# Kernel optimization log

Hardware: AMD Instinct MI355X
Metric: run time of the kernel (lower is better)

The kernel has to match this reference:

```python
import jax, jax.numpy as jnp
import numpy as np

N, D, S, K = 4096, 256, 32, 4   # nodes, in_dim(=out_dim), subspace_dim, num_heads
ETA = 0.5
LAMBDA_SPARSE = 0.05
EDGE_P = 0.02  # graph density for the random adjacency mask


def setup_inputs() -> dict:
    key = jax.random.key(0)
    k1, k2, k3 = jax.random.split(key, 3)
    H = jax.random.normal(k1, (N, D), dtype=jnp.float32)
    # binary adjacency mask with self-loops, stored as float (matches torch usage)
    mask = (jax.random.uniform(k2, (N, N)) < EDGE_P).astype(jnp.float32)
    adj_mask = jnp.maximum(mask, jnp.eye(N, dtype=jnp.float32))
    # per-head orthonormal subspace bases U[k] = qr(randn(D,S)) -> [K, D, S]
    raw = jax.random.normal(k3, (K, D, S), dtype=jnp.float32)
    U, _ = jnp.linalg.qr(raw)
    log_precision = jnp.zeros((K, S), dtype=jnp.float32)
    threshold = jnp.full((D,), LAMBDA_SPARSE, dtype=jnp.float32)
    return {"H": H, "adj_mask": adj_mask, "U": U,
            "log_precision": log_precision, "threshold": threshold}


def reference(H, adj_mask, U, log_precision, threshold):
    s = U.shape[-1]
    inv_sqrt_s = 1.0 / jnp.sqrt(jnp.asarray(s, dtype=H.dtype))
    neg = (1.0 - adj_mask) * (-1e9)  # [N, N] additive mask

    # scan over heads keeps peak memory at one [N,N] score matrix at a time
    def head_step(agg, xs):
        Uk, lpk = xs                       # [D,S], [S]
        Z = H @ Uk                         # [N,S]  (= Zk^T in the torch code)
        Zs = Z * jnp.exp(lpk)              # precision-scaled
        scores = (Zs @ Z.T) * inv_sqrt_s + neg   # [N,N]
        alpha = jax.nn.softmax(scores, axis=-1)
        agg = agg + (alpha @ Z) @ Uk.T     # [N,D] == (Uk @ (Zk @ alpha^T))^T
        return agg, None

    agg, _ = jax.lax.scan(head_step, jnp.zeros_like(H), (U, log_precision))
    H_half = H + ETA * agg                 # in_dim == out_dim -> no proj

    # soft threshold
    H_out = jnp.sign(H_half) * jax.nn.relu(jnp.abs(H_half) - threshold[None, :])

    # orthogonality loss: sum_k ||Uk^T Uk - I||_F^2 + sum_{k<l} ||Uk^T Ul||_F^2
    C = jnp.einsum('kda,ldb->klab', U, U)  # [K,K,S,S] gram blocks (K,S small)
    Kh = U.shape[0]
    I = jnp.eye(s, dtype=U.dtype)
    diag_blocks = C[jnp.arange(Kh), jnp.arange(Kh)]          # [K,S,S]
    orth_loss = ((diag_blocks - I) ** 2).sum()
    upper = jnp.triu(jnp.ones((Kh, Kh), dtype=U.dtype), 1)[:, :, None, None]
    orth_loss = orth_loss + ((C ** 2) * upper).sum()
    return H_out, orth_loss
```

## Files before the change

kernel.cpp:

```cpp
#include <hip/hip_runtime.h>
#include <math.h>

constexpr int NN = 4096;
constexpr int DD = 256;
constexpr int SS = 32;
constexpr int KK = 4;
constexpr int MAXN = 192;
constexpr int SEGMAX = 96;
constexpr float ETA = 0.5f;

#define MEMFENCE() __asm__ volatile("" ::: "memory")

typedef float nfloat4 __attribute__((ext_vector_type(4)));

__device__ __forceinline__ float4 ntload4(const float4* p) {
  nfloat4 v = __builtin_nontemporal_load((const nfloat4*)p);
  float4 r; r.x = v.x; r.y = v.y; r.z = v.z; r.w = v.w;
  return r;
}

__global__ __launch_bounds__(256) void prep_kernel(
    const float* __restrict__ H, const float* __restrict__ U,
    const float* __restrict__ lp, float* __restrict__ Z,
    float* __restrict__ elp, float* __restrict__ lossp) {
  __shared__ float Hl[16][DD];
  __shared__ float red[4];
  const int tid = threadIdx.x;

  if (blockIdx.x < 1024) {
    const int k = blockIdx.x & 3;
    const int n0 = (blockIdx.x >> 2) * 16;

    const float4* H4 = (const float4*)(H + (size_t)n0 * DD);
    float4* Hl4 = (float4*)&Hl[0][0];
    for (int i = tid; i < 16 * DD / 4; i += 256) Hl4[i] = H4[i];
    __syncthreads();

    const int s = tid & 31;
    const int n_l = (tid >> 5) & 7;
    const float* Uk = U + (size_t)k * DD * SS;
    float acc0 = 0.f, acc1 = 0.f;
#pragma unroll 4
    for (int dq = 0; dq < DD / 4; dq++) {
      const float4 h0 = Hl4[n_l * (DD / 4) + dq];
      const float4 h1 = Hl4[(n_l + 8) * (DD / 4) + dq];
      const float u0 = Uk[(4 * dq + 0) * SS + s];
      const float u1 = Uk[(4 * dq + 1) * SS + s];
      const float u2 = Uk[(4 * dq + 2) * SS + s];
      const float u3 = Uk[(4 * dq + 3) * SS + s];
      acc0 += h0.x * u0 + h0.y * u1 + h0.z * u2 + h0.w * u3;
      acc1 += h1.x * u0 + h1.y * u1 + h1.z * u2 + h1.w * u3;
    }
    Z[((size_t)k * NN + n0 + n_l) * SS + s] = acc0;
    Z[((size_t)k * NN + n0 + n_l + 8) * SS + s] = acc1;
  } else {
    const int pair = blockIdx.x - 1024;
    if (pair == 0 && tid < KK * SS) elp[tid] = expf(lp[tid]);
    const int pk[10] = {0, 0, 0, 0, 1, 1, 1, 2, 2, 3};
    const int pl[10] = {0, 1, 2, 3, 1, 2, 3, 2, 3, 3};
    const int k = pk[pair], l = pl[pair];
    const int b = tid & 31;
    const int a0 = tid >> 5;
    float acc[4] = {0.f, 0.f, 0.f, 0.f};
    for (int d = 0; d < DD; d++) {
      const float ub = U[((size_t)l * DD + d) * SS + b];
#pragma unroll
      for (int j = 0; j < 4; j++)
        acc[j] += U[((size_t)k * DD + d) * SS + a0 + 8 * j] * ub;
    }
    float tot = 0.f;
#pragma unroll
    for (int j = 0; j < 4; j++) {
      const float cv = acc[j] - ((k == l && (a0 + 8 * j) == b) ? 1.0f : 0.0f);
      tot += cv * cv;
    }
#pragma unroll
    for (int off = 32; off >= 1; off >>= 1) tot += __shfl_xor(tot, off);
    if ((tid & 63) == 0) red[tid >> 6] = tot;
    __syncthreads();
    if (tid == 0) lossp[pair] = red[0] + red[1] + red[2] + red[3];
  }
}

__global__ __launch_bounds__(256) void attn_row(
    const float* __restrict__ mask, const float* __restrict__ Z,
    const float* __restrict__ elp, const float* __restrict__ lossp,
    float* __restrict__ AO, float* __restrict__ loss) {
  const int tid = threadIdx.x;
  const int wv = tid >> 6;
  const int lane = tid & 63;
  const int row = blockIdx.x;

  __shared__ int segn[4][SEGMAX];
  __shared__ int segc[4];
  __shared__ int nbr[MAXN];

  if (blockIdx.x == 0 && tid == 0) {
    float t = 0.f;
#pragma unroll
    for (int i = 0; i < 10; i++) t += lossp[i];
    loss[0] = t;
  }

  const float4* m4 = (const float4*)(mask + (size_t)row * NN);
  const unsigned long long lt = (1ULL << lane) - 1ULL;
  int cnt = 0;
#pragma unroll
  for (int it = 0; it < 4; it++) {
    const int i = wv * 256 + it * 64 + lane;
    const float4 v = ntload4(&m4[i]);
    unsigned long long b;
    b = __ballot(v.x > 0.5f);
    if (v.x > 0.5f) { const int p = cnt + (int)__popcll(b & lt); if (p < SEGMAX) segn[wv][p] = 4 * i; }
    cnt += (int)__popcll(b);
    b = __ballot(v.y > 0.5f);
    if (v.y > 0.5f) { const int p = cnt + (int)__popcll(b & lt); if (p < SEGMAX) segn[wv][p] = 4 * i + 1; }
    cnt += (int)__popcll(b);
    b = __ballot(v.z > 0.5f);
    if (v.z > 0.5f) { const int p = cnt + (int)__popcll(b & lt); if (p < SEGMAX) segn[wv][p] = 4 * i + 2; }
    cnt += (int)__popcll(b);
    b = __ballot(v.w > 0.5f);
    if (v.w > 0.5f) { const int p = cnt + (int)__popcll(b & lt); if (p < SEGMAX) segn[wv][p] = 4 * i + 3; }
    cnt += (int)__popcll(b);
  }
  if (lane == 0) segc[wv] = min(cnt, SEGMAX);
  MEMFENCE();
  __syncthreads();

  const int c0 = segc[0], c1 = segc[1], c2 = segc[2], c3 = segc[3];
  const int offs[4] = {0, c0, c0 + c1, c0 + c1 + c2};
  const int c = min(c0 + c1 + c2 + c3, MAXN);
  const int myc = segc[wv];
  const int myoff = offs[wv];
  for (int i = lane; i < myc; i += 64) {
    const int p = myoff + i;
    if (p < MAXN) nbr[p] = segn[wv][i];
  }
  MEMFENCE();
  __syncthreads();

  const int k = wv;
  const int p_sub = lane >> 3;
  const int sq = lane & 7;
  const float inv_sqrt_s = 0.17677669529663687f;
  const float* Zk = Z + (size_t)k * NN * SS;

  float4 q4;
  {
    const float4 a = ((const float4*)(Z + ((size_t)k * NN + row) * SS))[sq];
    const float4 e = ((const float4*)(elp + k * SS))[sq];
    q4.x = a.x * e.x; q4.y = a.y * e.y; q4.z = a.z * e.z; q4.w = a.w * e.w;
  }

  float m = -3.0e38f;
  float wsum = 0.f;
  float4 o4 = {0.f, 0.f, 0.f, 0.f};

  bool aA = p_sub < c, aB = (p_sub + 8) < c;
  float4 zA = {0.f, 0.f, 0.f, 0.f}, zB = {0.f, 0.f, 0.f, 0.f};
  if (aA) zA = ((const float4*)(Zk + (size_t)nbr[p_sub] * SS))[sq];
  if (aB) zB = ((const float4*)(Zk + (size_t)nbr[p_sub + 8] * SS))[sq];

  for (int p0 = 0; p0 < c; p0 += 16) {
    const int pa_n = p0 + 16 + p_sub;
    const int pb_n = pa_n + 8;
    const bool aA_n = pa_n < c, aB_n = pb_n < c;
    float4 zA_n = {0.f, 0.f, 0.f, 0.f}, zB_n = {0.f, 0.f, 0.f, 0.f};
    if (aA_n) zA_n = ((const float4*)(Zk + (size_t)nbr[pa_n] * SS))[sq];
    if (aB_n) zB_n = ((const float4*)(Zk + (size_t)nbr[pb_n] * SS))[sq];

    float dA = q4.x * zA.x + q4.y * zA.y + q4.z * zA.z + q4.w * zA.w;
    float dB = q4.x * zB.x + q4.y * zB.y + q4.z * zB.z + q4.w * zB.w;
    dA += __shfl_xor(dA, 1); dB += __shfl_xor(dB, 1);
    dA += __shfl_xor(dA, 2); dB += __shfl_xor(dB, 2);
    dA += __shfl_xor(dA, 4); dB += __shfl_xor(dB, 4);
    dA = aA ? dA * inv_sqrt_s : -3.0e38f;
    dB = aB ? dB * inv_sqrt_s : -3.0e38f;
    float cm = fmaxf(dA, dB);
    cm = fmaxf(cm, __shfl_xor(cm, 8));
    cm = fmaxf(cm, __shfl_xor(cm, 16));
    cm = fmaxf(cm, __shfl_xor(cm, 32));
    const float mn = fmaxf(m, cm);
    const float sc = __expf(m - mn);
    m = mn;
    const float wA = __expf(dA - m);
    const float wB = __expf(dB - m);
    o4.x = o4.x * sc + wA * zA.x + wB * zB.x;
    o4.y = o4.y * sc + wA * zA.y + wB * zB.y;
    o4.z = o4.z * sc + wA * zA.z + wB * zB.z;
    o4.w = o4.w * sc + wA * zA.w + wB * zB.w;
    wsum = wsum * sc + wA + wB;

    zA = zA_n; zB = zB_n; aA = aA_n; aB = aB_n;
  }
#pragma unroll
  for (int off = 8; off <= 32; off <<= 1) {
    o4.x += __shfl_xor(o4.x, off);
    o4.y += __shfl_xor(o4.y, off);
    o4.z += __shfl_xor(o4.z, off);
    o4.w += __shfl_xor(o4.w, off);
    wsum += __shfl_xor(wsum, off);
  }
  const float invl = 1.0f / wsum;
  if (p_sub == 0) {
    float4 o;
    o.x = o4.x * invl; o.y = o4.y * invl; o.z = o4.z * invl; o.w = o4.w * invl;
    ((float4*)AO)[(size_t)row * (KK * SS / 4) + k * 8 + sq] = o;
  }
}

__global__ __launch_bounds__(256) void epilogue_kernel(
    const float* __restrict__ H, const float* __restrict__ U,
    const float* __restrict__ thr, const float* __restrict__ AO,
    float* __restrict__ Hout) {
  __shared__ float AOl[4][KK * SS];
  const int tid = threadIdx.x;
  const int r0 = blockIdx.x * 4;

  const float4* AO4 = (const float4*)(AO + (size_t)r0 * KK * SS);
  float4* AOl4 = (float4*)&AOl[0][0];
  if (tid < 128) AOl4[tid] = AO4[tid];
  __syncthreads();

  const int d = tid;
  float acc[4] = {0.f, 0.f, 0.f, 0.f};
  const float4* U4 = (const float4*)U;
#pragma unroll
  for (int k = 0; k < KK; k++) {
    const int ubase = (k * DD + d) * (SS / 4);
#pragma unroll
    for (int sq = 0; sq < SS / 4; sq++) {
      const float4 u = U4[ubase + sq];
#pragma unroll
      for (int r = 0; r < 4; r++) {
        const float4 a = AOl4[r * (KK * SS / 4) + k * (SS / 4) + sq];
        acc[r] += u.x * a.x + u.y * a.y + u.z * a.z + u.w * a.w;
      }
    }
  }
  const float tv = thr[d];
#pragma unroll
  for (int r = 0; r < 4; r++) {
    const float h = __builtin_nontemporal_load(&H[(size_t)(r0 + r) * DD + d]) + ETA * acc[r];
    const float ab = fabsf(h) - tv;
    const float o = (ab > 0.0f) ? copysignf(ab, h) : 0.0f;
    __builtin_nontemporal_store(o, &Hout[(size_t)(r0 + r) * DD + d]);
  }
}

extern "C" void kernel_launch(void* const* d_in, const int* in_sizes, int n_in,
                              void* d_out, int out_size, void* d_ws, size_t ws_size,
                              hipStream_t stream) {
  const float* H    = (const float*)d_in[0];
  const float* mask = (const float*)d_in[1];
  const float* U    = (const float*)d_in[2];
  const float* lp   = (const float*)d_in[3];
  const float* thr  = (const float*)d_in[4];

  float* Hout = (float*)d_out;
  float* loss = Hout + (size_t)NN * DD;

  float* Z     = (float*)d_ws;
  float* AO    = Z + (size_t)KK * NN * SS;
  float* elp   = AO + (size_t)NN * KK * SS;
  float* lossp = elp + KK * SS;

  prep_kernel<<<1034, 256, 0, stream>>>(H, U, lp, Z, elp, lossp);
  attn_row<<<NN, 256, 0, stream>>>(mask, Z, elp, lossp, AO, loss);
  epilogue_kernel<<<NN / 4, 256, 0, stream>>>(H, U, thr, AO, Hout);
}
```

Before: 165.7 us.

## Fuse attention and epilogue kernels, processing four rows per block

The attention and epilogue kernels are merged. Each block now loops over four rows, computes their per-head attention outputs into shared memory, then does the U projection and soft threshold in the same block. This removes one kernel launch and the global AO round trip. In exchange each block handles four rows serially, so there are a quarter as many blocks and each row's neighbour gather and softmax run one after another with less latency hiding. The orthogonality-loss gram loop is also rewritten to use float4 loads of U.

Result: no change. 164.4 us (-0.8%).

```diff
diff --git a/kernel.cpp b/kernel.cpp
--- a/kernel.cpp
+++ b/kernel.cpp
@@ -12,7 +12,6 @@
 #define MEMFENCE() __asm__ volatile("" ::: "memory")
 
 typedef float nfloat4 __attribute__((ext_vector_type(4)));
-
 __device__ __forceinline__ float4 ntload4(const float4* p) {
   nfloat4 v = __builtin_nontemporal_load((const nfloat4*)p);
   float4 r; r.x = v.x; r.y = v.y; r.z = v.z; r.w = v.w;
@@ -61,19 +60,21 @@
     const int k = pk[pair], l = pl[pair];
     const int b = tid & 31;
     const int a0 = tid >> 5;
-    float acc[4] = {0.f, 0.f, 0.f, 0.f};
+    float4 acc = {0.f, 0.f, 0.f, 0.f};
+    const float4* Uk4 = (const float4*)(U + (size_t)k * DD * SS);
+    const float* Ul = U + (size_t)l * DD * SS;
     for (int d = 0; d < DD; d++) {
-      const float ub = U[((size_t)l * DD + d) * SS + b];
-#pragma unroll
-      for (int j = 0; j < 4; j++)
-        acc[j] += U[((size_t)k * DD + d) * SS + a0 + 8 * j] * ub;
-    }
-    float tot = 0.f;
-#pragma unroll
-    for (int j = 0; j < 4; j++) {
-      const float cv = acc[j] - ((k == l && (a0 + 8 * j) == b) ? 1.0f : 0.0f);
-      tot += cv * cv;
-    }
+      const float ub = Ul[(size_t)d * SS + b];
+      const float4 ua = Uk4[d * (SS / 4) + a0];
+      acc.x += ua.x * ub; acc.y += ua.y * ub;
+      acc.z += ua.z * ub; acc.w += ua.w * ub;
+    }
+    const int abase = 4 * a0;
+    float cvx = acc.x - ((k == l && abase + 0 == b) ? 1.0f : 0.0f);
+    float cvy = acc.y - ((k == l && abase + 1 == b) ? 1.0f : 0.0f);
+    float cvz = acc.z - ((k == l && abase + 2 == b) ? 1.0f : 0.0f);
+    float cvw = acc.w - ((k == l && abase + 3 == b) ? 1.0f : 0.0f);
+    float tot = cvx * cvx + cvy * cvy + cvz * cvz + cvw * cvw;
 #pragma unroll
     for (int off = 32; off >= 1; off >>= 1) tot += __shfl_xor(tot, off);
     if ((tid & 63) == 0) red[tid >> 6] = tot;
@@ -82,169 +83,171 @@
   }
 }
 
-__global__ __launch_bounds__(256) void attn_row(
+__global__ __launch_bounds__(256) void attn_epi(
     const float* __restrict__ mask, const float* __restrict__ Z,
     const float* __restrict__ elp, const float* __restrict__ lossp,
-    float* __restrict__ AO, float* __restrict__ loss) {
+    const float* __restrict__ H, const float* __restrict__ U,
+    const float* __restrict__ thr, float* __restrict__ Hout,
+    float* __restrict__ loss) {
   const int tid = threadIdx.x;
   const int wv = tid >> 6;
   const int lane = tid & 63;
-  const int row = blockIdx.x;
+  const int bid = blockIdx.x;
 
   __shared__ int segn[4][SEGMAX];
   __shared__ int segc[4];
   __shared__ int nbr[MAXN];
-
-  if (blockIdx.x == 0 && tid == 0) {
+  __shared__ float AOl[4][KK * SS];
+
+  if (bid == 0 && tid == 0) {
     float t = 0.f;
 #pragma unroll
     for (int i = 0; i < 10; i++) t += lossp[i];
     loss[0] = t;
   }
 
-  const float4* m4 = (const float4*)(mask + (size_t)row * NN);
-  const unsigned long long lt = (1ULL << lane) - 1ULL;
-  int cnt = 0;
-#pragma unroll
-  for (int it = 0; it < 4; it++) {
-    const int i = wv * 256 + it * 64 + lane;
-    const float4 v = ntload4(&m4[i]);
-    unsigned long long b;
-    b = __ballot(v.x > 0.5f);
-    if (v.x > 0.5f) { const int p = cnt + (int)__popcll(b & lt); if (p < SEGMAX) segn[wv][p] = 4 * i; }
-    cnt += (int)__popcll(b);
-    b = __ballot(v.y > 0.5f);
-    if (v.y > 0.5f) { const int p = cnt + (int)__popcll(b & lt); if (p < SEGMAX) segn[wv][p] = 4 * i + 1; }
-    cnt += (int)__popcll(b);
-    b = __ballot(v.z > 0.5f);
-    if (v.z > 0.5f) { const int p = cnt + (int)__popcll(b & lt); if (p < SEGMAX) segn[wv][p] = 4 * i + 2; }
-    cnt += (int)__popcll(b);
-    b = __ballot(v.w > 0.5f);
-    if (v.w > 0.5f) { const int p = cnt + (int)__popcll(b & lt); if (p < SEGMAX) segn[wv][p] = 4 * i + 3; }
-    cnt += (int)__popcll(b);
-  }
-  if (lane == 0) segc[wv] = min(cnt, SEGMAX);
-  MEMFENCE();
-  __syncthreads();
-
-  const int c0 = segc[0], c1 = segc[1], c2 = segc[2], c3 = segc[3];
-  const int offs[4] = {0, c0, c0 + c1, c0 + c1 + c2};
-  const int c = min(c0 + c1 + c2 + c3, MAXN);
-  const int myc = segc[wv];
-  const int myoff = offs[wv];
-  for (int i = lane; i < myc; i += 64) {
-    const int p = myoff + i;
-    if (p < MAXN) nbr[p] = segn[wv][i];
-  }
-  MEMFENCE();
-  __syncthreads();
-
-  const int k = wv;
   const int p_sub = lane >> 3;
   const int sq = lane & 7;
   const float inv_sqrt_s = 0.17677669529663687f;
+  const unsigned long long lt = (1ULL << lane) - 1ULL;
+  const int k = wv;
   const float* Zk = Z + (size_t)k * NN * SS;
 
-  float4 q4;
+  for (int r = 0; r < 4; r++) {
+    const int row = bid * 4 + r;
+    if (r) __syncthreads();
+
+    const float4* m4 = (const float4*)(mask + (size_t)row * NN);
+    int cnt = 0;
+#pragma unroll
+    for (int it = 0; it < 4; it++) {
+      const int i = wv * 256 + it * 64 + lane;
+      const float4 v = ntload4(&m4[i]);
+      unsigned long long bb;
+      bb = __ballot(v.x > 0.5f);
+      if (v.x > 0.5f) { const int p = cnt + (int)__popcll(bb & lt); if (p < SEGMAX) segn[wv][p] = 4 * i; }
+      cnt += (int)__popcll(bb);
+      bb = __ballot(v.y > 0.5f);
+      if (v.y > 0.5f) { const int p = cnt + (int)__popcll(bb & lt); if (p < SEGMAX) segn[wv][p] = 4 * i + 1; }
+      cnt += (int)__popcll(bb);
+      bb = __ballot(v.z > 0.5f);
+      if (v.z > 0.5f) { const int p = cnt + (int)__popcll(bb & lt); if (p < SEGMAX) segn[wv][p] = 4 * i + 2; }
+      cnt += (int)__popcll(bb);
+      bb = __ballot(v.w > 0.5f);
+      if (v.w > 0.5f) { const int p = cnt + (int)__popcll(bb & lt); if (p < SEGMAX) segn[wv][p] = 4 * i + 3; }
+      cnt += (int)__popcll(bb);
+    }
+    if (lane == 0) segc[wv] = min(cnt, SEGMAX);
+    MEMFENCE();
+    __syncthreads();
+
+    const int c0 = segc[0], c1 = segc[1], c2 = segc[2], c3 = segc[3];
+    const int offs[4] = {0, c0, c0 + c1, c0 + c1 + c2};
+    const int c = min(c0 + c1 + c2 + c3, MAXN);
+    const int myc = segc[wv];
+    const int myoff = offs[wv];
+    for (int i = lane; i < myc; i += 64) {
+      const int p = myoff + i;
+      if (p < MAXN) nbr[p] = segn[wv][i];
+    }
+    MEMFENCE();
+    __syncthreads();
+
+    float4 q4;
+    {
+      const float4 a = ((const float4*)(Z + ((size_t)k * NN + row) * SS))[sq];
+      const float4 e = ((const float4*)(elp + k * SS))[sq];
+      q4.x = a.x * e.x; q4.y = a.y * e.y; q4.z = a.z * e.z; q4.w = a.w * e.w;
+    }
+
+    float m = -3.0e38f;
+    float wsum = 0.f;
+    float4 o4 = {0.f, 0.f, 0.f, 0.f};
+
+    bool aA = p_sub < c, aB = (p_sub + 8) < c;
+    float4 zA = {0.f, 0.f, 0.f, 0.f}, zB = {0.f, 0.f, 0.f, 0.f};
+    if (aA) zA = ((const float4*)(Zk + (size_t)nbr[p_sub] * SS))[sq];
+    if (aB) zB = ((const float4*)(Zk + (size_t)nbr[p_sub + 8] * SS))[sq];
+
+    for (int p0 = 0; p0 < c; p0 += 16) {
+      const int pa_n = p0 + 16 + p_sub;
+      const int pb_n = pa_n + 8;
+      const bool aA_n = pa_n < c, aB_n = pb_n < c;
+      float4 zA_n = {0.f, 0.f, 0.f, 0.f}, zB_n = {0.f, 0.f, 0.f, 0.f};
+      if (aA_n) zA_n = ((const float4*)(Zk + (size_t)nbr[pa_n] * SS))[sq];
+      if (aB_n) zB_n = ((const float4*)(Zk + (size_t)nbr[pb_n] * SS))[sq];
+
+      float dA = q4.x * zA.x + q4.y * zA.y + q4.z * zA.z + q4.w * zA.w;
+      float dB = q4.x * zB.x + q4.y * zB.y + q4.z * zB.z + q4.w * zB.w;
+      dA += __shfl_xor(dA, 1); dB += __shfl_xor(dB, 1);
+      dA += __shfl_xor(dA, 2); dB += __shfl_xor(dB, 2);
+      dA += __shfl_xor(dA, 4); dB += __shfl_xor(dB, 4);
+      dA = aA ? dA * inv_sqrt_s : -3.0e38f;
+      dB = aB ? dB * inv_sqrt_s : -3.0e38f;
+      float cm = fmaxf(dA, dB);
+      cm = fmaxf(cm, __shfl_xor(cm, 8));
+      cm = fmaxf(cm, __shfl_xor(cm, 16));
+      cm = fmaxf(cm, __shfl_xor(cm, 32));
+      const float mn = fmaxf(m, cm);
+      const float sc = __expf(m - mn);
+      m = mn;
+      const float wA = __expf(dA - m);
+      const float wB = __expf(dB - m);
+      o4.x = o4.x * sc + wA * zA.x + wB * zB.x;
+      o4.y = o4.y * sc + wA * zA.y + wB * zB.y;
+      o4.z = o4.z * sc + wA * zA.z + wB * zB.z;
+      o4.w = o4.w * sc + wA * zA.w + wB * zB.w;
+      wsum = wsum * sc + wA + wB;
+
+      zA = zA_n; zB = zB_n; aA = aA_n; aB = aB_n;
+    }
+#pragma unroll
+    for (int off = 8; off <= 32; off <<= 1) {
+      o4.x += __shfl_xor(o4.x, off);
+      o4.y += __shfl_xor(o4.y, off);
+      o4.z += __shfl_xor(o4.z, off);
+      o4.w += __shfl_xor(o4.w, off);
+      wsum += __shfl_xor(wsum, off);
+    }
+    const float invl = 1.0f / wsum;
+    if (p_sub == 0) {
+      float4 o;
+      o.x = o4.x * invl; o.y = o4.y * invl;
+      o.z = o4.z * invl; o.w = o4.w * invl;
+      ((float4*)&AOl[r][0])[k * 8 + sq] = o;
+    }
+  }
+  MEMFENCE();
+  __syncthreads();
+
   {
-    const float4 a = ((const float4*)(Z + ((size_t)k * NN + row) * SS))[sq];
-    const float4 e = ((const float4*)(elp + k * SS))[sq];
-    q4.x = a.x * e.x; q4.y = a.y * e.y; q4.z = a.z * e.z; q4.w = a.w * e.w;
-  }
-
-  float m = -3.0e38f;
-  float wsum = 0.f;
-  float4 o4 = {0.f, 0.f, 0.f, 0.f};
-
-  bool aA = p_sub < c, aB = (p_sub + 8) < c;
-  float4 zA = {0.f, 0.f, 0.f, 0.f}, zB = {0.f, 0.f, 0.f, 0.f};
-  if (aA) zA = ((const float4*)(Zk + (size_t)nbr[p_sub] * SS))[sq];
-  if (aB) zB = ((const float4*)(Zk + (size_t)nbr[p_sub + 8] * SS))[sq];
-
-  for (int p0 = 0; p0 < c; p0 += 16) {
-    const int pa_n = p0 + 16 + p_sub;
-    const int pb_n = pa_n + 8;
-    const bool aA_n = pa_n < c, aB_n = pb_n < c;
-    float4 zA_n = {0.f, 0.f, 0.f, 0.f}, zB_n = {0.f, 0.f, 0.f, 0.f};
-    if (aA_n) zA_n = ((const float4*)(Zk + (size_t)nbr[pa_n] * SS))[sq];
-    if (aB_n) zB_n = ((const float4*)(Zk + (size_t)nbr[pb_n] * SS))[sq];
-
-    float dA = q4.x * zA.x + q4.y * zA.y + q4.z * zA.z + q4.w * zA.w;
-    float dB = q4.x * zB.x + q4.y * zB.y + q4.z * zB.z + q4.w * zB.w;
-    dA += __shfl_xor(dA, 1); dB += __shfl_xor(dB, 1);
-    dA += __shfl_xor(dA, 2); dB += __shfl_xor(dB, 2);
-    dA += __shfl_xor(dA, 4); dB += __shfl_xor(dB, 4);
-    dA = aA ? dA * inv_sqrt_s : -3.0e38f;
-    dB = aB ? dB * inv_sqrt_s : -3.0e38f;
-    float cm = fmaxf(dA, dB);
-    cm = fmaxf(cm, __shfl_xor(cm, 8));
-    cm = fmaxf(cm, __shfl_xor(cm, 16));
-    cm = fmaxf(cm, __shfl_xor(cm, 32));
-    const float mn = fmaxf(m, cm);
-    const float sc = __expf(m - mn);
-    m = mn;
-    const float wA = __expf(dA - m);
-    const float wB = __expf(dB - m);
-    o4.x = o4.x * sc + wA * zA.x + wB * zB.x;
-    o4.y = o4.y * sc + wA * zA.y + wB * zB.y;
-    o4.z = o4.z * sc + wA * zA.z + wB * zB.z;
-    o4.w = o4.w * sc + wA * zA.w + wB * zB.w;
-    wsum = wsum * sc + wA + wB;
-
-    zA = zA_n; zB = zB_n; aA = aA_n; aB = aB_n;
-  }
-#pragma unroll
-  for (int off = 8; off <= 32; off <<= 1) {
-    o4.x += __shfl_xor(o4.x, off);
-    o4.y += __shfl_xor(o4.y, off);
-    o4.z += __shfl_xor(o4.z, off);
-    o4.w += __shfl_xor(o4.w, off);
-    wsum += __shfl_xor(wsum, off);
-  }
-  const float invl = 1.0f / wsum;
-  if (p_sub == 0) {
-    float4 o;
-    o.x = o4.x * invl; o.y = o4.y * invl; o.z = o4.z * invl; o.w = o4.w * invl;
-    ((float4*)AO)[(size_t)row * (KK * SS / 4) + k * 8 + sq] = o;
-  }
-}
-
-__global__ __launch_bounds__(256) void epilogue_kernel(
-    const float* __restrict__ H, const float* __restrict__ U,
-    const float* __restrict__ thr, const float* __restrict__ AO,
-    float* __restrict__ Hout) {
-  __shared__ float AOl[4][KK * SS];
-  const int tid = threadIdx.x;
-  const int r0 = blockIdx.x * 4;
-
-  const float4* AO4 = (const float4*)(AO + (size_t)r0 * KK * SS);
-  float4* AOl4 = (float4*)&AOl[0][0];
-  if (tid < 128) AOl4[tid] = AO4[tid];
-  __syncthreads();
-
-  const int d = tid;
-  float acc[4] = {0.f, 0.f, 0.f, 0.f};
-  const float4* U4 = (const float4*)U;
-#pragma unroll
-  for (int k = 0; k < KK; k++) {
-    const int ubase = (k * DD + d) * (SS / 4);
-#pragma unroll
-    for (int sq = 0; sq < SS / 4; sq++) {
-      const float4 u = U4[ubase + sq];
-#pragma unroll
-      for (int r = 0; r < 4; r++) {
-        const float4 a = AOl4[r * (KK * SS / 4) + k * (SS / 4) + sq];
-        acc[r] += u.x * a.x + u.y * a.y + u.z * a.z + u.w * a.w;
+    const int r0 = bid * 4;
+    const int d = tid;
+    float acc[4] = {0.f, 0.f, 0.f, 0.f};
+    const float4* U4 = (const float4*)U;
+    const float4* AOl4 = (const float4*)&AOl[0][0];
+#pragma unroll
+    for (int kk = 0; kk < KK; kk++) {
+      const int ubase = (kk * DD + d) * (SS / 4);
+#pragma unroll
+      for (int sq2 = 0; sq2 < SS / 4; sq2++) {
+        const float4 u = U4[ubase + sq2];
+#pragma unroll
+        for (int r = 0; r < 4; r++) {
+          const float4 a = AOl4[r * (KK * SS / 4) + kk * (SS / 4) + sq2];
+          acc[r] += u.x * a.x + u.y * a.y + u.z * a.z + u.w * a.w;
+        }
       }
     }
-  }
-  const float tv = thr[d];
-#pragma unroll
-  for (int r = 0; r < 4; r++) {
-    const float h = __builtin_nontemporal_load(&H[(size_t)(r0 + r) * DD + d]) + ETA * acc[r];
-    const float ab = fabsf(h) - tv;
-    const float o = (ab > 0.0f) ? copysignf(ab, h) : 0.0f;
-    __builtin_nontemporal_store(o, &Hout[(size_t)(r0 + r) * DD + d]);
+    const float tv = thr[d];
+#pragma unroll
+    for (int r = 0; r < 4; r++) {
+      const float h =
+          __builtin_nontemporal_load(&H[(size_t)(r0 + r) * DD + d]) + ETA * acc[r];
+      const float ab = fabsf(h) - tv;
+      const float o = (ab > 0.0f) ? copysignf(ab, h) : 0.0f;
+      __builtin_nontemporal_store(o, &Hout[(size_t)(r0 + r) * DD + d]);
+    }
   }
 }
 
@@ -261,11 +264,9 @@
   float* loss = Hout + (size_t)NN * DD;
 
   float* Z     = (float*)d_ws;
-  float* AO    = Z + (size_t)KK * NN * SS;
-  float* elp   = AO + (size_t)NN * KK * SS;
+  float* elp   = Z + (size_t)KK * NN * SS;
   float* lossp = elp + KK * SS;
 
   prep_kernel<<<1034, 256, 0, stream>>>(H, U, lp, Z, elp, lossp);
-  attn_row<<<NN, 256, 0, stream>>>(mask, Z, elp, lossp, AO, loss);
-  epilogue_kernel<<<NN / 4, 256, 0, stream>>>(H, U, thr, AO, Hout);
-}
+  attn_epi<<<NN / 4, 256, 0, stream>>>(mask, Z, elp, lossp, H, U, thr, Hout, loss);
+}
```
